# Kernel tuning notes

Measured on AMD Instinct MI355X. Metric: run time of the kernel, lower is better.

## Reference

```python
import jax, jax.numpy as jnp
import numpy as np

N, E = 50000, 1_000_000
IN_F, OUT_F = 128, 64
NEG_SLOPE = 0.2


def setup_inputs() -> dict:
    key = jax.random.key(0)
    k1, k2, k3, k4, k5 = jax.random.split(key, 5)
    x = jax.random.normal(k1, (N, IN_F), dtype=jnp.float32)
    edge_index = jax.random.randint(k2, (2, E), 0, N, dtype=jnp.int64)
    # xavier_uniform with gain=1.414 (as in the torch init)
    gain = 1.414
    bW = gain * np.sqrt(6.0 / (IN_F + OUT_F))
    W = jax.random.uniform(k3, (IN_F, OUT_F), jnp.float32, -bW, bW)
    ba = gain * np.sqrt(6.0 / (OUT_F + 1))
    a_src = jax.random.uniform(k4, (OUT_F, 1), jnp.float32, -ba, ba)
    a_dst = jax.random.uniform(k5, (OUT_F, 1), jnp.float32, -ba, ba)
    return {"x": x, "edge_index": edge_index, "W": W, "a_src": a_src, "a_dst": a_dst}


def reference(x, edge_index, W, a_src, a_dst):
    n = x.shape[0]
    Wh = x @ W                                  # [N, F_out]
    src = edge_index[0]
    dst = edge_index[1]
    # per-edge attention logits: (Wh[src] . a_src) + (Wh[dst] . a_dst)
    s_src = Wh @ a_src[:, 0]                    # [N]
    s_dst = Wh @ a_dst[:, 0]                    # [N]
    e = jax.nn.leaky_relu(s_src[src] + s_dst[dst], negative_slope=NEG_SLOPE)  # [E]
    e = jnp.exp(e - jnp.max(e))                 # global-max stabilized exp (matches torch code)
    denom = jax.ops.segment_sum(e, dst, num_segments=n) + 1e-16  # [N]
    alpha = e / denom[dst]                      # [E]  (dropout p=0 -> identity)
    out = jax.ops.segment_sum(Wh[src] * alpha[:, None], dst, num_segments=n)  # [N, F_out]
    return jax.nn.elu(out)
```

## Files before the change

kernel.cpp:

```cpp
#include <hip/hip_runtime.h>
#include <hip/hip_bf16.h>
#include <math.h>

#define NN 50000
#define NE 1000000
#define FIN 128
#define FOUT 64
#define NEG 0.2f

#define NB   2048
#define DPB  25
#define NBUSED 2000
#define TS   4096
#define NT   245
#define NTP  256
#define RCAP 1024
#define TILE_BLKS 245
#define GEMM_BLKS 391

using short8  = __attribute__((ext_vector_type(8))) short;
using floatx4 = __attribute__((ext_vector_type(4))) float;
using floatx2 = __attribute__((ext_vector_type(2))) float;

static __device__ __forceinline__ short f2bf(float f) {
    __hip_bfloat16 h = __float2bfloat16(f);
    return *(short*)&h;
}

__global__ __launch_bounds__(512) void k_front(
    const float* __restrict__ x, const float* __restrict__ W,
    const float* __restrict__ a_src, const float* __restrict__ a_dst,
    const int* __restrict__ ei,
    __hip_bfloat16* __restrict__ Whb, float* __restrict__ s_src,
    float* __restrict__ s_dst,
    unsigned* __restrict__ bdata, int* __restrict__ gofs_t)
{
    __shared__ int cnt[NB];
    __shared__ int cur[NB];
    __shared__ unsigned srt[TS];
    __shared__ int wsum[8];

    const int tid  = threadIdx.x;
    const int lane = tid & 63;
    const int wv   = tid >> 6;

    if (blockIdx.x >= TILE_BLKS) {
        const int col  = lane & 15;
        const int quad = lane >> 4;
        const int strip = (blockIdx.x - TILE_BLKS) * 8 + wv;
        if (strip >= NN / 16) return;
        const int row0 = strip * 16;

        short8 bfr[4][4];
        #pragma unroll
        for (int kk = 0; kk < 4; ++kk) {
            #pragma unroll
            for (int nt = 0; nt < 4; ++nt) {
                const float* wp = W + (kk * 32 + quad * 8) * FOUT + nt * 16 + col;
                #pragma unroll
                for (int j = 0; j < 8; ++j)
                    bfr[kk][nt][j] = f2bf(wp[j * FOUT]);
            }
        }

        floatx4 acc[4] = {{0.f,0.f,0.f,0.f},{0.f,0.f,0.f,0.f},
                          {0.f,0.f,0.f,0.f},{0.f,0.f,0.f,0.f}};

        const float* xrow = x + (size_t)(row0 + col) * FIN + quad * 8;
        #pragma unroll
        for (int kk = 0; kk < 4; ++kk) {
            const floatx4 u0 = __builtin_nontemporal_load(
                (const floatx4*)(xrow + kk * 32));
            const floatx4 u1 = __builtin_nontemporal_load(
                (const floatx4*)(xrow + kk * 32 + 4));
            short8 af;
            af[0] = f2bf(u0[0]); af[1] = f2bf(u0[1]);
            af[2] = f2bf(u0[2]); af[3] = f2bf(u0[3]);
            af[4] = f2bf(u1[0]); af[5] = f2bf(u1[1]);
            af[6] = f2bf(u1[2]); af[7] = f2bf(u1[3]);
            #pragma unroll
            for (int nt = 0; nt < 4; ++nt)
                acc[nt] = __builtin_amdgcn_mfma_f32_16x16x32_bf16(
                    af, bfr[kk][nt], acc[nt], 0, 0, 0);
        }

        const float av0 = a_src[col], av1 = a_src[16 + col];
        const float av2 = a_src[32 + col], av3 = a_src[48 + col];
        const float bv0 = a_dst[col], bv1 = a_dst[16 + col];
        const float bv2 = a_dst[32 + col], bv3 = a_dst[48 + col];

        float ps[4], pd[4];
        #pragma unroll
        for (int reg = 0; reg < 4; ++reg) {
            ps[reg] = acc[0][reg] * av0 + acc[1][reg] * av1
                    + acc[2][reg] * av2 + acc[3][reg] * av3;
            pd[reg] = acc[0][reg] * bv0 + acc[1][reg] * bv1
                    + acc[2][reg] * bv2 + acc[3][reg] * bv3;
        }

        #pragma unroll
        for (int nt = 0; nt < 4; ++nt)
            #pragma unroll
            for (int reg = 0; reg < 4; ++reg)
                Whb[(size_t)(row0 + quad * 4 + reg) * FOUT + nt * 16 + col] =
                    __float2bfloat16(acc[nt][reg]);

        #pragma unroll
        for (int off = 1; off < 16; off <<= 1) {
            #pragma unroll
            for (int reg = 0; reg < 4; ++reg) {
                ps[reg] += __shfl_xor(ps[reg], off);
                pd[reg] += __shfl_xor(pd[reg], off);
            }
        }
        if (col == 0) {
            #pragma unroll
            for (int reg = 0; reg < 4; ++reg) {
                s_src[row0 + quad * 4 + reg] = ps[reg];
                s_dst[row0 + quad * 4 + reg] = pd[reg];
            }
        }
        return;
    }

    const int tile = blockIdx.x;
    const int base = tile * TS;
    const int tcnt = (NE - base < TS) ? (NE - base) : TS;

    for (int i = tid; i < NB; i += 512) cnt[i] = 0;
    __syncthreads();

    unsigned pk[8];
    #pragma unroll
    for (int j = 0; j < 8; ++j) {
        const int i = j * 512 + tid;
        if (i < tcnt) {
            const int e = base + i;
            const unsigned s = (unsigned)__builtin_nontemporal_load(ei + e);
            const unsigned d = (unsigned)__builtin_nontemporal_load(ei + NE + e);
            pk[j] = (s << 16) | d;
            atomicAdd(&cnt[d / DPB], 1);
        } else pk[j] = 0xFFFFFFFFu;
    }
    __syncthreads();

    {
        const int i0 = tid * 4;
        const int v0 = cnt[i0], v1 = cnt[i0 + 1];
        const int v2 = cnt[i0 + 2], v3 = cnt[i0 + 3];
        const int s = v0 + v1 + v2 + v3;
        int inc = s;
        #pragma unroll
        for (int off = 1; off < 64; off <<= 1) {
            const int t = __shfl_up(inc, off);
            if (lane >= off) inc += t;
        }
        if (lane == 63) wsum[wv] = inc;
        __syncthreads();
        int wb = 0;
        #pragma unroll
        for (int w = 0; w < 7; ++w) if (w < wv) wb += wsum[w];
        const int excl = wb + inc - s;
        cur[i0]     = excl;
        cur[i0 + 1] = excl + v0;
        cur[i0 + 2] = excl + v0 + v1;
        cur[i0 + 3] = excl + v0 + v1 + v2;
        int* gt = gofs_t + tile;
        gt[(size_t)i0 * NTP]       = excl;
        gt[(size_t)(i0 + 1) * NTP] = excl + v0;
        gt[(size_t)(i0 + 2) * NTP] = excl + v0 + v1;
        gt[(size_t)(i0 + 3) * NTP] = excl + v0 + v1 + v2;
    }
    __syncthreads();

    #pragma unroll
    for (int j = 0; j < 8; ++j) {
        if (pk[j] != 0xFFFFFFFFu) {
            const int b = (int)(pk[j] & 0xffffu) / DPB;
            const int pos = atomicAdd(&cur[b], 1);
            srt[pos] = pk[j];
        }
    }
    __syncthreads();

    for (int i = tid; i < tcnt; i += 512)
        bdata[base + i] = srt[i];
}

__global__ __launch_bounds__(256) void k_sortgather(
    const int* __restrict__ gofs_t, const unsigned* __restrict__ bdata,
    const float* __restrict__ s_src, const float* __restrict__ s_dst,
    const __hip_bfloat16* __restrict__ Whb, float* __restrict__ out)
{
    __shared__ unsigned raw[RCAP];
    __shared__ uint2 pes[RCAP];
    __shared__ float sdl[32];
    __shared__ int cnt[32];
    __shared__ int ofs2[33];
    __shared__ int cur[32];
    __shared__ int wsum[4];

    const int b = (blockIdx.x & 7) * 250 + (blockIdx.x >> 3);
    const int tid = threadIdx.x;
    const int lane = tid & 63;
    const int wv = tid >> 6;
    const int d0 = b * DPB;

    if (tid < 32) {
        cnt[tid] = 0;
        sdl[tid] = (tid < DPB) ? s_dst[d0 + tid] : 0.f;
    }

    int c = 0, o = 0;
    if (tid < NT) {
        o = gofs_t[(size_t)b * NTP + tid];
        c = gofs_t[(size_t)(b + 1) * NTP + tid] - o;
    }
    int inc = c;
    #pragma unroll
    for (int off = 1; off < 64; off <<= 1) {
        const int t = __shfl_up(inc, off);
        if (lane >= off) inc += t;
    }
    if (lane == 63) wsum[wv] = inc;
    __syncthreads();
    int wb = 0;
    #pragma unroll
    for (int w = 0; w < 3; ++w) if (w < wv) wb += wsum[w];
    const int segbase = wb + inc - c;
    int tot = wsum[0] + wsum[1] + wsum[2] + wsum[3];
    if (tot > RCAP) tot = RCAP;

    {
        const unsigned* bsrc = bdata + (size_t)tid * TS + o;
        int lim = RCAP - segbase; if (lim > c) lim = c; if (lim < 0) lim = 0;
        for (int k = 0; k < lim; ++k)
            raw[segbase + k] = bsrc[k];
    }
    __syncthreads();

    for (int i = tid; i < tot; i += 256)
        atomicAdd(&cnt[(int)(raw[i] & 0xffffu) - d0], 1);
    __syncthreads();

    if (tid < 32) {
        const int cc = (tid < DPB) ? cnt[tid] : 0;
        int in2 = cc;
        #pragma unroll
        for (int off = 1; off < 32; off <<= 1) {
            const int t = __shfl_up(in2, off);
            if (tid >= off) in2 += t;
        }
        ofs2[tid + 1] = in2;
        if (tid == 0) ofs2[0] = 0;
        cur[tid] = in2 - cc;
    }
    __syncthreads();

    for (int i = tid; i < tot; i += 256) {
        const unsigned p = raw[i];
        const int j = (int)(p & 0xffffu) - d0;
        const int pos = atomicAdd(&cur[j], 1);
        float v = s_src[p >> 16] + sdl[j];
        v = (v > 0.f) ? v : NEG * v;
        pes[pos] = make_uint2((p & 0xffff0000u) >> 9,
                              __float_as_uint(__expf(v)));
    }
    __syncthreads();

    const int h  = lane >> 5;
    const int l5 = lane & 31;
    const char* wbase = (const char*)Whb + (l5 << 2);
    for (int j = wv; j < DPB; j += 4) {
        const int d = d0 + j;
        const int beg = ofs2[j];
        const int end = ofs2[j + 1];
        float a0 = 0.f, a1 = 0.f, dacc = 0.f;
        int i = beg;
        for (; i + 8 <= end; i += 8) {
            #pragma unroll
            for (int k = 0; k < 4; ++k) {
                const uint2 q = pes[i + 2 * k + h];
                const float ev = __uint_as_float(q.y);
                const unsigned u = *(const unsigned*)(wbase + q.x);
                const float f0 = __uint_as_float(u << 16);
                const float f1 = __uint_as_float(u & 0xffff0000u);
                a0 = fmaf(ev, f0, a0);
                a1 = fmaf(ev, f1, a1);
                dacc += ev;
            }
        }
        for (; i + 2 <= end; i += 2) {
            const uint2 q = pes[i + h];
            const float ev = __uint_as_float(q.y);
            const unsigned u = *(const unsigned*)(wbase + q.x);
            a0 = fmaf(ev, __uint_as_float(u << 16), a0);
            a1 = fmaf(ev, __uint_as_float(u & 0xffff0000u), a1);
            dacc += ev;
        }
        if (i < end && h == 0) {
            const uint2 q = pes[i];
            const float ev = __uint_as_float(q.y);
            const unsigned u = *(const unsigned*)(wbase + q.x);
            a0 = fmaf(ev, __uint_as_float(u << 16), a0);
            a1 = fmaf(ev, __uint_as_float(u & 0xffff0000u), a1);
            dacc += ev;
        }
        a0 += __shfl_xor(a0, 32);
        a1 += __shfl_xor(a1, 32);
        dacc += __shfl_xor(dacc, 32);
        if (h == 0) {
            const float rd = 1.f / (dacc + 1e-16f);
            float r0 = a0 * rd, r1 = a1 * rd;
            r0 = (r0 > 0.f) ? r0 : expm1f(r0);
            r1 = (r1 > 0.f) ? r1 : expm1f(r1);
            floatx2 rr; rr[0] = r0; rr[1] = r1;
            __builtin_nontemporal_store(
                rr, (floatx2*)(out + (size_t)d * FOUT) + l5);
        }
    }
}

extern "C" void kernel_launch(void* const* d_in, const int* in_sizes, int n_in,
                              void* d_out, int out_size, void* d_ws, size_t ws_size,
                              hipStream_t stream)
{
    const float* x     = (const float*)d_in[0];
    const int*   ei    = (const int*)d_in[1];
    const float* W     = (const float*)d_in[2];
    const float* a_src = (const float*)d_in[3];
    const float* a_dst = (const float*)d_in[4];
    float* out = (float*)d_out;

    float* ws    = (float*)d_ws;
    __hip_bfloat16* Whb = (__hip_bfloat16*)ws;
    float* s_src = ws + (size_t)NN * FOUT / 2;
    float* s_dst = s_src + NN;
    int*   gofs_t = (int*)(s_dst + NN);
    unsigned* bdata = (unsigned*)(gofs_t + (size_t)NB * NTP);

    k_front<<<TILE_BLKS + GEMM_BLKS, 512, 0, stream>>>(
        x, W, a_src, a_dst, ei, Whb, s_src, s_dst, bdata, gofs_t);
    k_sortgather<<<NBUSED, 256, 0, stream>>>(gofs_t, bdata, s_src, s_dst,
                                             Whb, out);
}
```

Baseline: 125.1 us.

## Stage W in swizzled LDS, store tile offsets row-major, gather 8-byte rows

The GEMM blocks now convert W to bf16 once into a swizzled shared-memory layout and load B fragments as 16-byte vectors, replacing many strided scalar global loads per wave. The per-tile bucket offsets are written tile-major with one int4 store instead of four strided scattered stores, which moves the strided access to the reader side. The gather loop has each lane fetch 4 bf16 features (8 bytes) and processes 4 edges per wave step, so fewer, wider loads are issued, at the cost of an extra shuffle-reduction stage. The shared-memory arrays are merged into one union buffer so both block roles fit.

```diff
diff --git a/kernel.cpp b/kernel.cpp
--- a/kernel.cpp
+++ b/kernel.cpp
@@ -13,7 +13,6 @@
 #define NBUSED 2000
 #define TS   4096
 #define NT   245
-#define NTP  256
 #define RCAP 1024
 #define TILE_BLKS 245
 #define GEMM_BLKS 391
@@ -33,11 +32,9 @@
     const int* __restrict__ ei,
     __hip_bfloat16* __restrict__ Whb, float* __restrict__ s_src,
     float* __restrict__ s_dst,
-    unsigned* __restrict__ bdata, int* __restrict__ gofs_t)
+    unsigned* __restrict__ bdata, int* __restrict__ gofs)
 {
-    __shared__ int cnt[NB];
-    __shared__ int cur[NB];
-    __shared__ unsigned srt[TS];
+    __shared__ int shmem_i[8192];
     __shared__ int wsum[8];
 
     const int tid  = threadIdx.x;
@@ -45,6 +42,16 @@
     const int wv   = tid >> 6;
 
     if (blockIdx.x >= TILE_BLKS) {
+        short* Wbt = (short*)shmem_i;
+
+        #pragma unroll
+        for (int rep = 0; rep < 16; ++rep) {
+            const int e = rep * 512 + tid;
+            const int k = e >> 6, n = e & 63;
+            Wbt[n * 128 + (((k >> 3) ^ (n & 15)) << 3) + (k & 7)] = f2bf(W[e]);
+        }
+        __syncthreads();
+
         const int col  = lane & 15;
         const int quad = lane >> 4;
         const int strip = (blockIdx.x - TILE_BLKS) * 8 + wv;
@@ -56,10 +63,9 @@
         for (int kk = 0; kk < 4; ++kk) {
             #pragma unroll
             for (int nt = 0; nt < 4; ++nt) {
-                const float* wp = W + (kk * 32 + quad * 8) * FOUT + nt * 16 + col;
-                #pragma unroll
-                for (int j = 0; j < 8; ++j)
-                    bfr[kk][nt][j] = f2bf(wp[j * FOUT]);
+                const int n = nt * 16 + col;
+                bfr[kk][nt] = *(const short8*)(
+                    Wbt + n * 128 + ((((kk << 2) + quad) ^ (n & 15)) << 3));
             }
         }
 
@@ -122,6 +128,10 @@
         }
         return;
     }
+
+    int* cnt = shmem_i;
+    int* cur = shmem_i + NB;
+    unsigned* srt = (unsigned*)(shmem_i + 2 * NB);
 
     const int tile = blockIdx.x;
     const int base = tile * TS;
@@ -165,11 +175,8 @@
         cur[i0 + 1] = excl + v0;
         cur[i0 + 2] = excl + v0 + v1;
         cur[i0 + 3] = excl + v0 + v1 + v2;
-        int* gt = gofs_t + tile;
-        gt[(size_t)i0 * NTP]       = excl;
-        gt[(size_t)(i0 + 1) * NTP] = excl + v0;
-        gt[(size_t)(i0 + 2) * NTP] = excl + v0 + v1;
-        gt[(size_t)(i0 + 3) * NTP] = excl + v0 + v1 + v2;
+        *(int4*)(gofs + (size_t)tile * NB + i0) =
+            make_int4(excl, excl + v0, excl + v0 + v1, excl + v0 + v1 + v2);
     }
     __syncthreads();
 
@@ -188,7 +195,7 @@
 }
 
 __global__ __launch_bounds__(256) void k_sortgather(
-    const int* __restrict__ gofs_t, const unsigned* __restrict__ bdata,
+    const int* __restrict__ gofs, const unsigned* __restrict__ bdata,
     const float* __restrict__ s_src, const float* __restrict__ s_dst,
     const __hip_bfloat16* __restrict__ Whb, float* __restrict__ out)
 {
@@ -213,8 +220,9 @@
 
     int c = 0, o = 0;
     if (tid < NT) {
-        o = gofs_t[(size_t)b * NTP + tid];
-        c = gofs_t[(size_t)(b + 1) * NTP + tid] - o;
+        const int* gp = gofs + (size_t)tid * NB + b;
+        o = gp[0];
+        c = gp[1] - o;
     }
     int inc = c;
     #pragma unroll
@@ -268,55 +276,52 @@
     }
     __syncthreads();
 
-    const int h  = lane >> 5;
-    const int l5 = lane & 31;
-    const char* wbase = (const char*)Whb + (l5 << 2);
+    const int q4 = lane >> 4;
+    const int l4 = lane & 15;
+    const char* wbase = (const char*)Whb + (l4 << 3);
     for (int j = wv; j < DPB; j += 4) {
         const int d = d0 + j;
         const int beg = ofs2[j];
         const int end = ofs2[j + 1];
-        float a0 = 0.f, a1 = 0.f, dacc = 0.f;
+        float a0 = 0.f, a1 = 0.f, a2 = 0.f, a3 = 0.f, dacc = 0.f;
         int i = beg;
+        #define GBODY(idx)                                                 \
+            {                                                              \
+                const uint2 q = pes[idx];                                  \
+                const float ev = __uint_as_float(q.y);                     \
+                const uint2 u = *(const uint2*)(wbase + q.x);              \
+                a0 = fmaf(ev, __uint_as_float(u.x << 16), a0);             \
+                a1 = fmaf(ev, __uint_as_float(u.x & 0xffff0000u), a1);     \
+                a2 = fmaf(ev, __uint_as_float(u.y << 16), a2);             \
+                a3 = fmaf(ev, __uint_as_float(u.y & 0xffff0000u), a3);     \
+                dacc += ev;                                                \
+            }
         for (; i + 8 <= end; i += 8) {
-            #pragma unroll
-            for (int k = 0; k < 4; ++k) {
-                const uint2 q = pes[i + 2 * k + h];
-                const float ev = __uint_as_float(q.y);
-                const unsigned u = *(const unsigned*)(wbase + q.x);
-                const float f0 = __uint_as_float(u << 16);
-                const float f1 = __uint_as_float(u & 0xffff0000u);
-                a0 = fmaf(ev, f0, a0);
-                a1 = fmaf(ev, f1, a1);
-                dacc += ev;
-            }
-        }
-        for (; i + 2 <= end; i += 2) {
-            const uint2 q = pes[i + h];
-            const float ev = __uint_as_float(q.y);
-            const unsigned u = *(const unsigned*)(wbase + q.x);
-            a0 = fmaf(ev, __uint_as_float(u << 16), a0);
-            a1 = fmaf(ev, __uint_as_float(u & 0xffff0000u), a1);
-            dacc += ev;
-        }
-        if (i < end && h == 0) {
-            const uint2 q = pes[i];
-            const float ev = __uint_as_float(q.y);
-            const unsigned u = *(const unsigned*)(wbase + q.x);
-            a0 = fmaf(ev, __uint_as_float(u << 16), a0);
-            a1 = fmaf(ev, __uint_as_float(u & 0xffff0000u), a1);
-            dacc += ev;
-        }
-        a0 += __shfl_xor(a0, 32);
-        a1 += __shfl_xor(a1, 32);
+            GBODY(i + q4)
+            GBODY(i + 4 + q4)
+        }
+        for (; i + 4 <= end; i += 4)
+            GBODY(i + q4)
+        if (i < end && q4 < end - i)
+            GBODY(i + q4)
+        #undef GBODY
+        a0 += __shfl_xor(a0, 16); a1 += __shfl_xor(a1, 16);
+        a2 += __shfl_xor(a2, 16); a3 += __shfl_xor(a3, 16);
+        dacc += __shfl_xor(dacc, 16);
+        a0 += __shfl_xor(a0, 32); a1 += __shfl_xor(a1, 32);
+        a2 += __shfl_xor(a2, 32); a3 += __shfl_xor(a3, 32);
         dacc += __shfl_xor(dacc, 32);
-        if (h == 0) {
+        if (lane < 16) {
             const float rd = 1.f / (dacc + 1e-16f);
             float r0 = a0 * rd, r1 = a1 * rd;
+            float r2 = a2 * rd, r3 = a3 * rd;
             r0 = (r0 > 0.f) ? r0 : expm1f(r0);
             r1 = (r1 > 0.f) ? r1 : expm1f(r1);
-            floatx2 rr; rr[0] = r0; rr[1] = r1;
+            r2 = (r2 > 0.f) ? r2 : expm1f(r2);
+            r3 = (r3 > 0.f) ? r3 : expm1f(r3);
+            floatx4 rr; rr[0] = r0; rr[1] = r1; rr[2] = r2; rr[3] = r3;
             __builtin_nontemporal_store(
-                rr, (floatx2*)(out + (size_t)d * FOUT) + l5);
+                rr, (floatx4*)(out + (size_t)d * FOUT) + l4);
         }
     }
 }
@@ -336,11 +341,11 @@
     __hip_bfloat16* Whb = (__hip_bfloat16*)ws;
     float* s_src = ws + (size_t)NN * FOUT / 2;
     float* s_dst = s_src + NN;
-    int*   gofs_t = (int*)(s_dst + NN);
-    unsigned* bdata = (unsigned*)(gofs_t + (size_t)NB * NTP);
+    int*   gofs  = (int*)(s_dst + NN);
+    unsigned* bdata = (unsigned*)(gofs + (size_t)NT * NB);
 
     k_front<<<TILE_BLKS + GEMM_BLKS, 512, 0, stream>>>(
-        x, W, a_src, a_dst, ei, Whb, s_src, s_dst, bdata, gofs_t);
-    k_sortgather<<<NBUSED, 256, 0, stream>>>(gofs_t, bdata, s_src, s_dst,
+        x, W, a_src, a_dst, ei, Whb, s_src, s_dst, bdata, gofs);
+    k_sortgather<<<NBUSED, 256, 0, stream>>>(gofs, bdata, s_src, s_dst,
                                              Whb, out);
 }
```

Measured after the change: 118.1 us. -5.6%, faster.
